# Performance work log

Measured on AMD Instinct MI355X. Metric: run time of the kernel, lower is better.

## Reference

```python
import jax, jax.numpy as jnp
import numpy as np

N_BASIS = 5  # identity, transpose, diag-embed(diag), row-sum broadcast, total-sum broadcast


def eq2to2_ops(x):
    """x: [B, d, n, n] -> [B, 5, d, n, n] equivariant basis ops (sums normalized by n, n^2)."""
    n = x.shape[-1]
    eye = jnp.eye(n, dtype=x.dtype)
    xt = jnp.swapaxes(x, -1, -2)
    diag = jnp.diagonal(x, axis1=-2, axis2=-1)            # [B, d, n]
    diag_emb = diag[..., :, None] * eye                   # [B, d, n, n]
    row = jnp.broadcast_to(x.sum(-1, keepdims=True) / n, x.shape)
    tot = jnp.broadcast_to(x.sum((-2, -1), keepdims=True) / (n * n), x.shape)
    return jnp.stack([x, xt, diag_emb, row, tot], axis=1)


def eq_layer(x, W, b):
    """x: [B, d_in, n, n]; W: [d_in, d_out, 5]; b: [d_out] -> [B, d_out, n, n]."""
    ops = eq2to2_ops(x)                                   # [B, 5, d_in, n, n]
    return jnp.einsum('bqdij,dsq->bsij', ops, W) + b[None, :, None, None]


def setup_inputs() -> dict:
    key = jax.random.key(0)
    ks = jax.random.split(key, 8)
    B, n, nin, nhid, ndechid, nout = 8, 256, 16, 32, 128, 1
    s = lambda fan: 1.0 / np.sqrt(fan)
    return {
        'x': jax.random.normal(ks[0], (B, n, nin), jnp.float32),
        'W1': jax.random.normal(ks[1], (2 * nin, nhid, N_BASIS), jnp.float32) * s(2 * nin * N_BASIS),
        'b1': jnp.zeros((nhid,), jnp.float32),
        'W2': jax.random.normal(ks[2], (nhid, nhid, N_BASIS), jnp.float32) * s(nhid * N_BASIS),
        'b2': jnp.zeros((nhid,), jnp.float32),
        'D1': jax.random.normal(ks[3], (nhid, ndechid), jnp.float32) * s(nhid),
        'db1': jnp.zeros((ndechid,), jnp.float32),
        'D2': jax.random.normal(ks[4], (ndechid, ndechid), jnp.float32) * s(ndechid),
        'db2': jnp.zeros((ndechid,), jnp.float32),
        'D3': jax.random.normal(ks[5], (ndechid, nout), jnp.float32) * s(ndechid),
        'db3': jnp.zeros((nout,), jnp.float32),
    }


def reference(x, W1, b1, W2, b2, D1, db1, D2, db2, D3, db3):
    B, n, d = x.shape
    eye = jnp.eye(n, dtype=x.dtype)
    # diag_embed(x.permute(0,2,1)) -> [B, d, n, n]
    x1 = jnp.swapaxes(x, 1, 2)[..., :, None] * eye
    # outer-product pairwise interactions -> [B, d, n, n]
    x2 = jnp.einsum('bid,bjd->bdij', x, x)
    h = jnp.concatenate([x1, x2], axis=1)                 # [B, 2d, n, n]
    h = jax.nn.relu(eq_layer(h, W1, b1))
    h = jax.nn.relu(eq_layer(h, W2, b2))
    h = jax.nn.relu(h.sum((-2, -1)))                      # [B, nhid]
    h = jax.nn.relu(h @ D1 + db1)
    h = jax.nn.relu(h @ D2 + db2)
    return h @ D3 + db3
```

## Files before the change

kernel.cpp:

```cpp
#include <hip/hip_runtime.h>
#include <hip/hip_bf16.h>


#define NB 8
#define NN 256
#define ND 16
#define NC 32
#define W1S (NC * 5)

using bf16x8 = __attribute__((ext_vector_type(8))) __bf16;
using f32x4  = __attribute__((ext_vector_type(4))) float;

#define MFMA(a, b, c) __builtin_amdgcn_mfma_f32_16x16x32_bf16((a), (b), (c), 0, 0, 0)

__global__ __launch_bounds__(256) void kB_pre(
    const float* __restrict__ x, const float* __restrict__ W1,
    const float* __restrict__ b1, const float* __restrict__ W2,
    float* __restrict__ S, float* __restrict__ T1,
    float* __restrict__ Tot1, float* __restrict__ G,
    float* __restrict__ W2dT, float* __restrict__ W2rT, float* __restrict__ W2tT,
    __bf16* __restrict__ A1wT, __bf16* __restrict__ WpT, __bf16* __restrict__ WmT)
{
    int b = blockIdx.x, t = threadIdx.x;
    __shared__ float part[16][ND + 1];
    __shared__ float sS[ND];
    const float* xb = x + b * NN * ND;

    { int i0 = t >> 4, d = t & 15; float p = 0.f;
      #pragma unroll
      for (int k = 0; k < 16; ++k) p += xb[(i0 + (k << 4)) * ND + d];
      part[i0][d] = p; }
    __syncthreads();
    if (t < ND) { float s = 0.f;
      #pragma unroll
      for (int k = 0; k < 16; ++k) s += part[k][t];
      sS[t] = s; S[b * ND + t] = s; }
    __syncthreads();
    if (t < NC) { int c = t; float tt = 0.f;
      #pragma unroll
      for (int d = 0; d < ND; ++d)
        tt += sS[d] * W1[d * W1S + c * 5 + 4]
            + sS[d] * sS[d] * W1[(ND + d) * W1S + c * 5 + 4];
      T1[b * NC + c] = tt * (1.f / 65536.f) + b1[c];
      Tot1[b * NC + c] = 0.f; G[b * NC + c] = 0.f; }
    if (b == 0) {
      for (int k = t; k < NC * ND; k += 256) {
        int c = k >> 4, d = k & 15;
        A1wT[k] = (__bf16)(W1[(ND + d) * W1S + c * 5 + 0]
                         + W1[(ND + d) * W1S + c * 5 + 1]);
      }
      for (int k = t; k < NC * NC; k += 256) {
        int s = k >> 5, c = k & 31;
        const float* w = W2 + c * W1S + s * 5;
        float w0 = w[0], w1 = w[1];
        WpT[k] = (__bf16)((w0 + w1) * 0.5f);
        WmT[k] = (__bf16)((w0 - w1) * 0.5f);
        W2dT[k] = w[2]; W2rT[k] = w[3]; W2tT[k] = w[4];
      }
    }
}

__global__ __launch_bounds__(256) void kC_rows(
    const float* __restrict__ x, const float* __restrict__ W1,
    const float* __restrict__ Sg, const float* __restrict__ T1g,
    const __bf16* __restrict__ A1wT,
    const float* __restrict__ W2dT, const float* __restrict__ W2rT,
    float* __restrict__ R1, float* __restrict__ Dg1, float* __restrict__ Tot1,
    float* __restrict__ CD2, float* __restrict__ CR2)
{
    const int i = blockIdx.x, b = blockIdx.y, t = threadIdx.x;
    __shared__ __align__(16) float  sX[NN][ND];
    __shared__ __align__(16) __bf16 sPA[NN][40];
    __shared__ __align__(16) __bf16 sBQ[NC][40];
    __shared__ float sS[ND], sDg[NC], sDiag[NC], sRow[NC];
    __shared__ float red[4][NC];

    { const float4* xb4 = (const float4*)(x + b * NN * ND);
      float4* sX4 = (float4*)&sX[0][0];
      #pragma unroll
      for (int kk = 0; kk < 4; ++kk) sX4[t + kk * 256] = xb4[t + kk * 256]; }
    if (t < ND) sS[t] = Sg[b * ND + t];
    for (int kk = 0; kk < 2; ++kk) {
      int idx = t + kk * 256; int c = idx >> 4, k = idx & 15;
      sBQ[c][k] = A1wT[idx];
    }
    __syncthreads();

    if (t < NC) {
      int c = t; float r = 0.f, dg = 0.f;
      #pragma unroll
      for (int d = 0; d < ND; ++d) {
        float xi = sX[i][d];
        r  += xi * W1[d * W1S + c * 5 + 3]
            + xi * sS[d] * W1[(ND + d) * W1S + c * 5 + 3];
        dg += xi * (W1[d * W1S + c * 5 + 0] + W1[d * W1S + c * 5 + 1]
                  + W1[d * W1S + c * 5 + 2])
            + xi * xi * W1[(ND + d) * W1S + c * 5 + 2];
      }
      r *= (1.f / 256.f);
      R1[(b * NN + i) * NC + c] = r;
      Dg1[(b * NN + i) * NC + c] = dg;
      sDg[c] = dg;
      sBQ[c][16] = (__bf16)(T1g[b * NC + c] + r);
      #pragma unroll
      for (int k = 17; k < 32; ++k) sBQ[c][k] = (__bf16)0.f;
    }
    {
      #pragma unroll
      for (int d = 0; d < ND; ++d) sPA[t][d] = (__bf16)(sX[i][d] * sX[t][d]);
      sPA[t][16] = (__bf16)1.f;
      #pragma unroll
      for (int k = 17; k < 32; ++k) sPA[t][k] = (__bf16)0.f;
    }
    __syncthreads();

    const int wv = t >> 6, ln = t & 63;
    const int m = ln & 15, quad = ln >> 4;
    const int c0 = m, c1 = m + 16;
    f32x4 zero = {0.f, 0.f, 0.f, 0.f};
    bf16x8 bq0 = *(const bf16x8*)&sBQ[c0][8 * quad];
    bf16x8 bq1 = *(const bf16x8*)&sBQ[c1][8 * quad];
    float rsum0 = 0.f, rsum1 = 0.f;
    #pragma unroll
    for (int gg = 0; gg < 4; ++gg) {
      int g = wv * 4 + gg;
      bf16x8 av = *(const bf16x8*)&sPA[g * 16 + m][8 * quad];
      f32x4 q0 = MFMA(av, bq0, zero);
      f32x4 q1 = MFMA(av, bq1, zero);
      #pragma unroll
      for (int r = 0; r < 4; ++r) {
        int pos = g * 16 + quad * 4 + r;
        float v0 = q0[r], v1 = q1[r];
        if (pos == i) { v0 += sDg[c0]; v1 += sDg[c1]; }
        float h0 = fmaxf(v0, 0.f), h1 = fmaxf(v1, 0.f);
        if (pos == i) { sDiag[c0] = h0; sDiag[c1] = h1; }
        rsum0 += h0; rsum1 += h1;
      }
    }
    rsum0 += __shfl_down(rsum0, 32, 64); rsum0 += __shfl_down(rsum0, 16, 64);
    rsum1 += __shfl_down(rsum1, 32, 64); rsum1 += __shfl_down(rsum1, 16, 64);
    if (ln < 16) { red[wv][ln] = rsum0; red[wv][ln + 16] = rsum1; }
    __syncthreads();
    if (t < NC) {
      float Row = red[0][t] + red[1][t] + red[2][t] + red[3][t];
      sRow[t] = Row;
      atomicAdd(&Tot1[b * NC + t], Row);
    }
    __syncthreads();
    if (t < NC) {
      int s = t; float cd = 0.f, cr = 0.f;
      #pragma unroll
      for (int c = 0; c < NC; ++c) {
        cd += sDiag[c] * W2dT[s * NC + c];
        cr += sRow[c]  * W2rT[s * NC + c];
      }
      CD2[(b * NN + i) * NC + s] = cd;
      CR2[(b * NN + i) * NC + s] = cr * (1.f / 256.f);
    }
}

__global__ __launch_bounds__(256) void kD_main(
    const float* __restrict__ x, const float* __restrict__ R1g,
    const float* __restrict__ Dg1g, const float* __restrict__ T1g,
    const float* __restrict__ CD2g, const float* __restrict__ CR2g,
    const float* __restrict__ Tot1g, const float* __restrict__ W2tT,
    const float* __restrict__ b2,
    const __bf16* __restrict__ A1wT, const __bf16* __restrict__ WpT,
    const __bf16* __restrict__ WmT,
    float* __restrict__ G)
{
    const int b = blockIdx.y, t = threadIdx.x;
    int TI = 0, rem = blockIdx.x;
    while (rem >= 16 - TI) { rem -= 16 - TI; ++TI; }
    const int TJ = TI + rem;
    const bool diagblk = (TI == TJ), mirror = (TI != TJ);

    __shared__ __align__(16) __bf16 sPA[NN][40];
    __shared__ __align__(16) __bf16 sV[NN][40];
    __shared__ __align__(16) __bf16 sBQ[NC][40];
    __shared__ __align__(16) __bf16 sWp[NC][40];
    __shared__ __align__(16) __bf16 sWm[NC][40];
    __shared__ float sXI[16][ND], sXJ[16][ND];
    __shared__ float sR1I[16][NC], sR1J[16][NC];
    __shared__ float sCR2I[16][NC], sCR2J[16][NC];
    __shared__ float sCD2I[16][NC], sDgI[16][NC];
    __shared__ float sCT2[NC];
    __shared__ float red[4][NC];

    { int r = t >> 4, d = t & 15;
      sXI[r][d] = x[(b * NN + TI * 16 + r) * ND + d];
      sXJ[r][d] = x[(b * NN + TJ * 16 + r) * ND + d]; }
    #pragma unroll
    for (int kk = 0; kk < 2; ++kk) {
      int idx = t + kk * 256; int r = idx >> 5, c = idx & 31;
      sR1I[r][c]  = R1g [(b * NN + TI * 16 + r) * NC + c];
      sR1J[r][c]  = R1g [(b * NN + TJ * 16 + r) * NC + c];
      sCR2I[r][c] = CR2g[(b * NN + TI * 16 + r) * NC + c];
      sCR2J[r][c] = CR2g[(b * NN + TJ * 16 + r) * NC + c];
      sCD2I[r][c] = CD2g[(b * NN + TI * 16 + r) * NC + c];
      sDgI[r][c]  = Dg1g[(b * NN + TI * 16 + r) * NC + c];
    }
    #pragma unroll
    for (int kk = 0; kk < 2; ++kk) {
      int idx = t + kk * 256; int c = idx >> 4, k = idx & 15;
      sBQ[c][k] = A1wT[idx];
    }
    if (t < NC) {
      sBQ[t][16] = (__bf16)T1g[b * NC + t];
      #pragma unroll
      for (int k = 17; k < 32; ++k) sBQ[t][k] = (__bf16)0.f;
    }
    #pragma unroll
    for (int kk = 0; kk < 4; ++kk) {
      int idx = t + kk * 256; int s = idx >> 5, c = idx & 31;
      sWp[s][c] = WpT[idx]; sWm[s][c] = WmT[idx];
    }
    if (t < NC) {
      float ct = 0.f;
      #pragma unroll
      for (int c = 0; c < NC; ++c) ct += Tot1g[b * NC + c] * W2tT[t * NC + c];
      sCT2[t] = ct * (1.f / 65536.f) + b2[t];
    }
    __syncthreads();

    {
      int ti = t >> 4, tj = t & 15;
      #pragma unroll
      for (int d = 0; d < ND; ++d) sPA[t][d] = (__bf16)(sXI[ti][d] * sXJ[tj][d]);
      sPA[t][16] = (__bf16)1.f;
      #pragma unroll
      for (int k = 17; k < 32; ++k) sPA[t][k] = (__bf16)0.f;
    }
    __syncthreads();

    const int wv = t >> 6, ln = t & 63;
    const int m = ln & 15, quad = ln >> 4;
    const int c0 = m, c1 = m + 16;
    f32x4 zero = {0.f, 0.f, 0.f, 0.f};

    {
      bf16x8 bq0 = *(const bf16x8*)&sBQ[c0][8 * quad];
      bf16x8 bq1 = *(const bf16x8*)&sBQ[c1][8 * quad];
      #pragma unroll
      for (int gg = 0; gg < 4; ++gg) {
        int g = wv * 4 + gg;
        bf16x8 av = *(const bf16x8*)&sPA[g * 16 + m][8 * quad];
        f32x4 q0 = MFMA(av, bq0, zero);
        f32x4 q1 = MFMA(av, bq1, zero);
        float r1i0 = sR1I[g][c0], r1i1 = sR1I[g][c1];
        #pragma unroll
        for (int r = 0; r < 4; ++r) {
          int tj = quad * 4 + r;
          float a0 = q0[r] + r1i0, b0 = q0[r] + sR1J[tj][c0];
          float a1v = q1[r] + r1i1, b1v = q1[r] + sR1J[tj][c1];
          if (diagblk && tj == g) {
            a0 += sDgI[g][c0]; b0 = a0;
            a1v += sDgI[g][c1]; b1v = a1v;
          }
          float hA0 = fmaxf(a0, 0.f), hB0 = fmaxf(b0, 0.f);
          float hA1 = fmaxf(a1v, 0.f), hB1 = fmaxf(b1v, 0.f);
          int pos = g * 16 + tj;
          sPA[pos][c0] = (__bf16)(hA0 + hB0);  sV[pos][c0] = (__bf16)(hA0 - hB0);
          sPA[pos][c1] = (__bf16)(hA1 + hB1);  sV[pos][c1] = (__bf16)(hA1 - hB1);
        }
      }
    }
    __syncthreads();

    const int s0 = m, s1 = m + 16;
    bf16x8 wp0 = *(const bf16x8*)&sWp[s0][8 * quad];
    bf16x8 wp1 = *(const bf16x8*)&sWp[s1][8 * quad];
    bf16x8 wm0 = *(const bf16x8*)&sWm[s0][8 * quad];
    bf16x8 wm1 = *(const bf16x8*)&sWm[s1][8 * quad];
    float ct0 = sCT2[s0], ct1 = sCT2[s1];
    float acc0 = 0.f, acc1 = 0.f;
    #pragma unroll
    for (int gg = 0; gg < 4; ++gg) {
      int g = wv * 4 + gg;
      bf16x8 ua = *(const bf16x8*)&sPA[g * 16 + m][8 * quad];
      bf16x8 va = *(const bf16x8*)&sV [g * 16 + m][8 * quad];
      f32x4 P0 = MFMA(ua, wp0, zero);
      f32x4 M0 = MFMA(va, wm0, zero);
      f32x4 P1 = MFMA(ua, wp1, zero);
      f32x4 M1 = MFMA(va, wm1, zero);
      float crI0 = sCR2I[g][s0], crI1 = sCR2I[g][s1];
      float cd0 = sCD2I[g][s0],  cd1 = sCD2I[g][s1];
      #pragma unroll
      for (int r = 0; r < 4; ++r) {
        int tj = quad * 4 + r;
        float a1 = P0[r] + M0[r] + crI0 + ct0;
        float a2 = P0[r] - M0[r] + sCR2J[tj][s0] + ct0;
        float b1v = P1[r] + M1[r] + crI1 + ct1;
        float b2v = P1[r] - M1[r] + sCR2J[tj][s1] + ct1;
        if (diagblk && tj == g) { a1 += cd0; b1v += cd1; }
        acc0 += fmaxf(a1, 0.f); acc1 += fmaxf(b1v, 0.f);
        if (mirror) { acc0 += fmaxf(a2, 0.f); acc1 += fmaxf(b2v, 0.f); }
      }
    }
    acc0 += __shfl_down(acc0, 32, 64); acc0 += __shfl_down(acc0, 16, 64);
    acc1 += __shfl_down(acc1, 32, 64); acc1 += __shfl_down(acc1, 16, 64);
    if (ln < 16) { red[wv][ln] = acc0; red[wv][ln + 16] = acc1; }
    __syncthreads();
    if (t < NC) {
      float v = red[0][t] + red[1][t] + red[2][t] + red[3][t];
      atomicAdd(&G[b * NC + t], v);
    }
}

__global__ __launch_bounds__(128) void k5_mlp(
    const float* __restrict__ G, const float* __restrict__ D1, const float* __restrict__ db1,
    const float* __restrict__ D2, const float* __restrict__ db2,
    const float* __restrict__ D3, const float* __restrict__ db3,
    float* __restrict__ out)
{
    int b = blockIdx.x, t = threadIdx.x;
    __shared__ float a[NC], h2s[128], r2[2];
    if (t < NC) a[t] = fmaxf(G[b * NC + t], 0.f);
    __syncthreads();
    float acc = db1[t];
    #pragma unroll
    for (int s = 0; s < NC; ++s) acc += a[s] * D1[s * 128 + t];
    float h2 = fmaxf(acc, 0.f);
    h2s[t] = h2;
    __syncthreads();
    float acc2 = db2[t];
    for (int u = 0; u < 128; ++u) acc2 += h2s[u] * D2[u * 128 + t];
    float h3 = fmaxf(acc2, 0.f);
    float v = h3 * D3[t];
    #pragma unroll
    for (int off = 32; off > 0; off >>= 1) v += __shfl_down(v, off, 64);
    if ((t & 63) == 0) r2[t >> 6] = v;
    __syncthreads();
    if (t == 0) out[b] = r2[0] + r2[1] + db3[0];
}

extern "C" void kernel_launch(void* const* d_in, const int* in_sizes, int n_in,
                              void* d_out, int out_size, void* d_ws, size_t ws_size,
                              hipStream_t stream)
{
    const float* x   = (const float*)d_in[0];
    const float* W1  = (const float*)d_in[1];
    const float* b1  = (const float*)d_in[2];
    const float* W2  = (const float*)d_in[3];
    const float* b2  = (const float*)d_in[4];
    const float* D1  = (const float*)d_in[5];
    const float* db1 = (const float*)d_in[6];
    const float* D2  = (const float*)d_in[7];
    const float* db2 = (const float*)d_in[8];
    const float* D3  = (const float*)d_in[9];
    const float* db3 = (const float*)d_in[10];
    float* out = (float*)d_out;

    float* w = (float*)d_ws;
    float* pS    = w; w += NB * ND;
    float* pT1   = w; w += NB * NC;
    float* pTot1 = w; w += NB * NC;
    float* pG    = w; w += NB * NC;
    float* pR1   = w; w += NB * NN * NC;
    float* pDg1  = w; w += NB * NN * NC;
    float* pCD2  = w; w += NB * NN * NC;
    float* pCR2  = w; w += NB * NN * NC;
    float* pW2d  = w; w += NC * NC;
    float* pW2r  = w; w += NC * NC;
    float* pW2t  = w; w += NC * NC;
    __bf16* bw = (__bf16*)w;
    __bf16* pA1wT = bw; bw += NC * ND;
    __bf16* pWpT  = bw; bw += NC * NC;
    __bf16* pWmT  = bw; bw += NC * NC;

    hipLaunchKernelGGL(kB_pre, dim3(NB), dim3(256), 0, stream,
                       x, W1, b1, W2, pS, pT1, pTot1, pG,
                       pW2d, pW2r, pW2t, pA1wT, pWpT, pWmT);
    hipLaunchKernelGGL(kC_rows, dim3(NN, NB), dim3(256), 0, stream,
                       x, W1, pS, pT1, pA1wT, pW2d, pW2r,
                       pR1, pDg1, pTot1, pCD2, pCR2);
    hipLaunchKernelGGL(kD_main, dim3(136, NB), dim3(256), 0, stream,
                       x, pR1, pDg1, pT1, pCD2, pCR2, pTot1, pW2t, b2,
                       pA1wT, pWpT, pWmT, pG);
    hipLaunchKernelGGL(k5_mlp, dim3(NB), dim3(128), 0, stream,
                       pG, D1, db1, D2, db2, D3, db3, out);
}
```

Before: 123.2 us.

## Fuse preprocessing into row kernel, batch 8 rows per block, replace atomics with partials

Removes the separate preprocessing kernel by recomputing column sums, T1 and the bf16 weight transforms inside the row and main kernels. The row kernel now handles 8 rows per block (32 blocks per batch instead of 256), looping over column chunks with MFMA. Global atomics are replaced by per-block partial buffers that later kernels reduce, which also drops the need to zero accumulators. This trades one kernel launch and the atomic traffic for redundant per-block weight and sum recomputation, plus fewer, longer-running row blocks.

```diff
diff --git a/kernel.cpp b/kernel.cpp
--- a/kernel.cpp
+++ b/kernel.cpp
@@ -6,185 +6,201 @@
 #define NN 256
 #define ND 16
 #define NC 32
-#define W1S (NC * 5)
+#define W1S 160
+#define W2S 160
 
 using bf16x8 = __attribute__((ext_vector_type(8))) __bf16;
 using f32x4  = __attribute__((ext_vector_type(4))) float;
 
 #define MFMA(a, b, c) __builtin_amdgcn_mfma_f32_16x16x32_bf16((a), (b), (c), 0, 0, 0)
 
-__global__ __launch_bounds__(256) void kB_pre(
+__global__ __launch_bounds__(256) void kC_rows(
     const float* __restrict__ x, const float* __restrict__ W1,
     const float* __restrict__ b1, const float* __restrict__ W2,
-    float* __restrict__ S, float* __restrict__ T1,
-    float* __restrict__ Tot1, float* __restrict__ G,
-    float* __restrict__ W2dT, float* __restrict__ W2rT, float* __restrict__ W2tT,
-    __bf16* __restrict__ A1wT, __bf16* __restrict__ WpT, __bf16* __restrict__ WmT)
+    float* __restrict__ T1g, float* __restrict__ R1, float* __restrict__ Dg1,
+    float* __restrict__ TotP, float* __restrict__ CD2, float* __restrict__ CR2)
 {
-    int b = blockIdx.x, t = threadIdx.x;
+    const int TI = blockIdx.x, b = blockIdx.y, t = threadIdx.x;
+    __shared__ __align__(16) float  sX[NN][ND + 1];
+    __shared__ __align__(16) __bf16 sP[NN][40];
+    __shared__ __align__(16) __bf16 sBQ[NC][48];
     __shared__ float part[16][ND + 1];
-    __shared__ float sS[ND];
-    const float* xb = x + b * NN * ND;
-
-    { int i0 = t >> 4, d = t & 15; float p = 0.f;
-      #pragma unroll
-      for (int k = 0; k < 16; ++k) p += xb[(i0 + (k << 4)) * ND + d];
-      part[i0][d] = p; }
-    __syncthreads();
-    if (t < ND) { float s = 0.f;
-      #pragma unroll
-      for (int k = 0; k < 16; ++k) s += part[k][t];
-      sS[t] = s; S[b * ND + t] = s; }
-    __syncthreads();
-    if (t < NC) { int c = t; float tt = 0.f;
-      #pragma unroll
-      for (int d = 0; d < ND; ++d)
-        tt += sS[d] * W1[d * W1S + c * 5 + 4]
-            + sS[d] * sS[d] * W1[(ND + d) * W1S + c * 5 + 4];
-      T1[b * NC + c] = tt * (1.f / 65536.f) + b1[c];
-      Tot1[b * NC + c] = 0.f; G[b * NC + c] = 0.f; }
-    if (b == 0) {
-      for (int k = t; k < NC * ND; k += 256) {
-        int c = k >> 4, d = k & 15;
-        A1wT[k] = (__bf16)(W1[(ND + d) * W1S + c * 5 + 0]
-                         + W1[(ND + d) * W1S + c * 5 + 1]);
-      }
-      for (int k = t; k < NC * NC; k += 256) {
-        int s = k >> 5, c = k & 31;
-        const float* w = W2 + c * W1S + s * 5;
-        float w0 = w[0], w1 = w[1];
-        WpT[k] = (__bf16)((w0 + w1) * 0.5f);
-        WmT[k] = (__bf16)((w0 - w1) * 0.5f);
-        W2dT[k] = w[2]; W2rT[k] = w[3]; W2tT[k] = w[4];
-      }
+    __shared__ float sS[ND], sT1[NC];
+    __shared__ float sRT[8][NC], sDgL[8][NC], sRow[8][NC], sDiag[8][NC];
+
+    const float* xg = x + b * NN * ND;
+    #pragma unroll
+    for (int kk = 0; kk < 16; ++kk) {
+        int idx = t + kk * 256;
+        sX[idx >> 4][idx & 15] = xg[idx];
+    }
+    #pragma unroll
+    for (int kk = 0; kk < 2; ++kk) {
+        int idx = t + kk * 256;
+        int c = idx >> 4, k = idx & 15;
+        sBQ[c][k] = (__bf16)(W1[(ND + k) * W1S + c * 5 + 0]
+                           + W1[(ND + k) * W1S + c * 5 + 1]);
+    }
+    #pragma unroll
+    for (int kk = 0; kk < 4; ++kk) {
+        int idx = t + kk * 256;
+        sBQ[idx >> 5][16 + (idx & 31)] = (__bf16)0.f;
+    }
+    {
+        uint32_t* z = (uint32_t*)&sP[0][0];
+        #pragma unroll
+        for (int kk = 0; kk < 8; ++kk) {
+            int idx = t + kk * 256;
+            z[(idx >> 3) * 20 + 8 + (idx & 7)] = 0u;
+        }
+    }
+    __syncthreads();
+
+    {
+        int rr = t >> 4, d = t & 15;
+        float p = 0.f;
+        #pragma unroll
+        for (int k = 0; k < 16; ++k) p += sX[rr + (k << 4)][d];
+        part[rr][d] = p;
+    }
+    __syncthreads();
+    if (t < ND) {
+        float s = 0.f;
+        #pragma unroll
+        for (int k = 0; k < 16; ++k) s += part[k][t];
+        sS[t] = s;
+    }
+    __syncthreads();
+    if (t < NC) {
+        int c = t; float tt = 0.f;
+        #pragma unroll
+        for (int d = 0; d < ND; ++d)
+            tt += sS[d] * W1[d * W1S + c * 5 + 4]
+                + sS[d] * sS[d] * W1[(ND + d) * W1S + c * 5 + 4];
+        float v = tt * (1.f / 65536.f) + b1[c];
+        sT1[c] = v;
+        if (TI == 0) T1g[b * NC + c] = v;
+    }
+    __syncthreads();
+    {
+        int i_l = t >> 5, c = t & 31;
+        int gi = TI * 8 + i_l;
+        float r = 0.f, dg = 0.f;
+        #pragma unroll
+        for (int d = 0; d < ND; ++d) {
+            float xi = sX[gi][d];
+            const float* wa = W1 + d * W1S + c * 5;
+            const float* wb = W1 + (ND + d) * W1S + c * 5;
+            r  += xi * wa[3] + xi * sS[d] * wb[3];
+            dg += xi * (wa[0] + wa[1] + wa[2]) + xi * xi * wb[2];
+        }
+        r *= (1.f / 256.f);
+        R1[(b * NN + gi) * NC + c] = r;
+        Dg1[(b * NN + gi) * NC + c] = dg;
+        sRT[i_l][c] = sT1[c] + r;
+        sDgL[i_l][c] = dg;
+    }
+
+    const int ln = t & 63, wv = t >> 6;
+    const int m = ln & 15, quad = ln >> 4;
+    bf16x8 bq0 = *(const bf16x8*)&sBQ[m][8 * quad];
+    bf16x8 bq1 = *(const bf16x8*)&sBQ[m + 16][8 * quad];
+    f32x4 zero = {0.f, 0.f, 0.f, 0.f};
+    float rs0[4] = {0.f, 0.f, 0.f, 0.f}, rs1[4] = {0.f, 0.f, 0.f, 0.f};
+    const int i_base = TI * 8;
+
+    for (int jg = 0; jg < 8; ++jg) {
+        __syncthreads();
+        {
+            int i_l = t >> 5, j_l = t & 31;
+            const float* xi = &sX[i_base + i_l][0];
+            const float* xj = &sX[jg * 32 + j_l][0];
+            bf16x8 v0, v1;
+            #pragma unroll
+            for (int d = 0; d < 8; ++d) v0[d] = (__bf16)(xi[d] * xj[d]);
+            #pragma unroll
+            for (int d = 0; d < 8; ++d) v1[d] = (__bf16)(xi[8 + d] * xj[8 + d]);
+            *(bf16x8*)&sP[t][0] = v0;
+            *(bf16x8*)&sP[t][8] = v1;
+        }
+        __syncthreads();
+        #pragma unroll
+        for (int gg = 0; gg < 4; ++gg) {
+            int g = wv * 4 + gg;
+            bf16x8 av = *(const bf16x8*)&sP[g * 16 + m][8 * quad];
+            f32x4 q0 = MFMA(av, bq0, zero);
+            f32x4 q1 = MFMA(av, bq1, zero);
+            int i_l = g >> 1;
+            int gi = i_base + i_l;
+            float rt0 = sRT[i_l][m], rt1 = sRT[i_l][m + 16];
+            int jb = jg * 32 + (g & 1) * 16 + quad * 4;
+            #pragma unroll
+            for (int r = 0; r < 4; ++r) {
+                float v0 = q0[r] + rt0, v1 = q1[r] + rt1;
+                bool dgf = (jb + r == gi);
+                if (dgf) { v0 += sDgL[i_l][m]; v1 += sDgL[i_l][m + 16]; }
+                float h0 = fmaxf(v0, 0.f), h1 = fmaxf(v1, 0.f);
+                if (dgf) { sDiag[i_l][m] = h0; sDiag[i_l][m + 16] = h1; }
+                rs0[gg] += h0; rs1[gg] += h1;
+            }
+        }
+    }
+    float a0 = rs0[0] + rs0[1], a1 = rs0[2] + rs0[3];
+    float b0 = rs1[0] + rs1[1], b1v = rs1[2] + rs1[3];
+    a0 += __shfl_down(a0, 32, 64);  a0 += __shfl_down(a0, 16, 64);
+    a1 += __shfl_down(a1, 32, 64);  a1 += __shfl_down(a1, 16, 64);
+    b0 += __shfl_down(b0, 32, 64);  b0 += __shfl_down(b0, 16, 64);
+    b1v += __shfl_down(b1v, 32, 64); b1v += __shfl_down(b1v, 16, 64);
+    __syncthreads();
+    if (ln < 16) {
+        sRow[wv * 2][ln] = a0;       sRow[wv * 2 + 1][ln] = a1;
+        sRow[wv * 2][ln + 16] = b0;  sRow[wv * 2 + 1][ln + 16] = b1v;
+    }
+    __syncthreads();
+    if (t < NC) {
+        float s = 0.f;
+        #pragma unroll
+        for (int i = 0; i < 8; ++i) s += sRow[i][t];
+        TotP[TI * (NB * NC) + b * NC + t] = s;
+    }
+    {
+        int i_l = t >> 5, s = t & 31;
+        int gi = i_base + i_l;
+        float cd = 0.f, cr = 0.f;
+        #pragma unroll
+        for (int c = 0; c < NC; ++c) {
+            cd += sDiag[i_l][c] * W2[c * W2S + s * 5 + 2];
+            cr += sRow[i_l][c]  * W2[c * W2S + s * 5 + 3];
+        }
+        CD2[(b * NN + gi) * NC + s] = cd;
+        CR2[(b * NN + gi) * NC + s] = cr * (1.f / 256.f);
     }
 }
 
-__global__ __launch_bounds__(256) void kC_rows(
+__global__ __launch_bounds__(256) void kD_main(
     const float* __restrict__ x, const float* __restrict__ W1,
-    const float* __restrict__ Sg, const float* __restrict__ T1g,
-    const __bf16* __restrict__ A1wT,
-    const float* __restrict__ W2dT, const float* __restrict__ W2rT,
-    float* __restrict__ R1, float* __restrict__ Dg1, float* __restrict__ Tot1,
-    float* __restrict__ CD2, float* __restrict__ CR2)
-{
-    const int i = blockIdx.x, b = blockIdx.y, t = threadIdx.x;
-    __shared__ __align__(16) float  sX[NN][ND];
-    __shared__ __align__(16) __bf16 sPA[NN][40];
-    __shared__ __align__(16) __bf16 sBQ[NC][40];
-    __shared__ float sS[ND], sDg[NC], sDiag[NC], sRow[NC];
-    __shared__ float red[4][NC];
-
-    { const float4* xb4 = (const float4*)(x + b * NN * ND);
-      float4* sX4 = (float4*)&sX[0][0];
-      #pragma unroll
-      for (int kk = 0; kk < 4; ++kk) sX4[t + kk * 256] = xb4[t + kk * 256]; }
-    if (t < ND) sS[t] = Sg[b * ND + t];
-    for (int kk = 0; kk < 2; ++kk) {
-      int idx = t + kk * 256; int c = idx >> 4, k = idx & 15;
-      sBQ[c][k] = A1wT[idx];
-    }
-    __syncthreads();
-
-    if (t < NC) {
-      int c = t; float r = 0.f, dg = 0.f;
-      #pragma unroll
-      for (int d = 0; d < ND; ++d) {
-        float xi = sX[i][d];
-        r  += xi * W1[d * W1S + c * 5 + 3]
-            + xi * sS[d] * W1[(ND + d) * W1S + c * 5 + 3];
-        dg += xi * (W1[d * W1S + c * 5 + 0] + W1[d * W1S + c * 5 + 1]
-                  + W1[d * W1S + c * 5 + 2])
-            + xi * xi * W1[(ND + d) * W1S + c * 5 + 2];
-      }
-      r *= (1.f / 256.f);
-      R1[(b * NN + i) * NC + c] = r;
-      Dg1[(b * NN + i) * NC + c] = dg;
-      sDg[c] = dg;
-      sBQ[c][16] = (__bf16)(T1g[b * NC + c] + r);
-      #pragma unroll
-      for (int k = 17; k < 32; ++k) sBQ[c][k] = (__bf16)0.f;
-    }
-    {
-      #pragma unroll
-      for (int d = 0; d < ND; ++d) sPA[t][d] = (__bf16)(sX[i][d] * sX[t][d]);
-      sPA[t][16] = (__bf16)1.f;
-      #pragma unroll
-      for (int k = 17; k < 32; ++k) sPA[t][k] = (__bf16)0.f;
-    }
-    __syncthreads();
-
-    const int wv = t >> 6, ln = t & 63;
-    const int m = ln & 15, quad = ln >> 4;
-    const int c0 = m, c1 = m + 16;
-    f32x4 zero = {0.f, 0.f, 0.f, 0.f};
-    bf16x8 bq0 = *(const bf16x8*)&sBQ[c0][8 * quad];
-    bf16x8 bq1 = *(const bf16x8*)&sBQ[c1][8 * quad];
-    float rsum0 = 0.f, rsum1 = 0.f;
-    #pragma unroll
-    for (int gg = 0; gg < 4; ++gg) {
-      int g = wv * 4 + gg;
-      bf16x8 av = *(const bf16x8*)&sPA[g * 16 + m][8 * quad];
-      f32x4 q0 = MFMA(av, bq0, zero);
-      f32x4 q1 = MFMA(av, bq1, zero);
-      #pragma unroll
-      for (int r = 0; r < 4; ++r) {
-        int pos = g * 16 + quad * 4 + r;
-        float v0 = q0[r], v1 = q1[r];
-        if (pos == i) { v0 += sDg[c0]; v1 += sDg[c1]; }
-        float h0 = fmaxf(v0, 0.f), h1 = fmaxf(v1, 0.f);
-        if (pos == i) { sDiag[c0] = h0; sDiag[c1] = h1; }
-        rsum0 += h0; rsum1 += h1;
-      }
-    }
-    rsum0 += __shfl_down(rsum0, 32, 64); rsum0 += __shfl_down(rsum0, 16, 64);
-    rsum1 += __shfl_down(rsum1, 32, 64); rsum1 += __shfl_down(rsum1, 16, 64);
-    if (ln < 16) { red[wv][ln] = rsum0; red[wv][ln + 16] = rsum1; }
-    __syncthreads();
-    if (t < NC) {
-      float Row = red[0][t] + red[1][t] + red[2][t] + red[3][t];
-      sRow[t] = Row;
-      atomicAdd(&Tot1[b * NC + t], Row);
-    }
-    __syncthreads();
-    if (t < NC) {
-      int s = t; float cd = 0.f, cr = 0.f;
-      #pragma unroll
-      for (int c = 0; c < NC; ++c) {
-        cd += sDiag[c] * W2dT[s * NC + c];
-        cr += sRow[c]  * W2rT[s * NC + c];
-      }
-      CD2[(b * NN + i) * NC + s] = cd;
-      CR2[(b * NN + i) * NC + s] = cr * (1.f / 256.f);
-    }
-}
-
-__global__ __launch_bounds__(256) void kD_main(
-    const float* __restrict__ x, const float* __restrict__ R1g,
-    const float* __restrict__ Dg1g, const float* __restrict__ T1g,
-    const float* __restrict__ CD2g, const float* __restrict__ CR2g,
-    const float* __restrict__ Tot1g, const float* __restrict__ W2tT,
-    const float* __restrict__ b2,
-    const __bf16* __restrict__ A1wT, const __bf16* __restrict__ WpT,
-    const __bf16* __restrict__ WmT,
-    float* __restrict__ G)
+    const float* __restrict__ W2, const float* __restrict__ b2,
+    const float* __restrict__ T1g, const float* __restrict__ R1g,
+    const float* __restrict__ Dg1g, const float* __restrict__ CD2g,
+    const float* __restrict__ CR2g, const float* __restrict__ TotP,
+    float* __restrict__ GP)
 {
     const int b = blockIdx.y, t = threadIdx.x;
     int TI = 0, rem = blockIdx.x;
     while (rem >= 16 - TI) { rem -= 16 - TI; ++TI; }
     const int TJ = TI + rem;
-    const bool diagblk = (TI == TJ), mirror = (TI != TJ);
+    const bool diagblk = (TI == TJ), mirror = !diagblk;
 
     __shared__ __align__(16) __bf16 sPA[NN][40];
     __shared__ __align__(16) __bf16 sV[NN][40];
-    __shared__ __align__(16) __bf16 sBQ[NC][40];
+    __shared__ __align__(16) __bf16 sBQ[NC][48];
     __shared__ __align__(16) __bf16 sWp[NC][40];
     __shared__ __align__(16) __bf16 sWm[NC][40];
-    __shared__ float sXI[16][ND], sXJ[16][ND];
+    __shared__ float sXI[16][ND + 1], sXJ[16][ND + 1];
     __shared__ float sR1I[16][NC], sR1J[16][NC];
     __shared__ float sCR2I[16][NC], sCR2J[16][NC];
     __shared__ float sCD2I[16][NC], sDgI[16][NC];
-    __shared__ float sCT2[NC];
+    __shared__ float sT1[NC], sTot[NC], sCT2[NC];
     __shared__ float red[4][NC];
 
     { int r = t >> 4, d = t & 15;
@@ -203,33 +219,49 @@
     #pragma unroll
     for (int kk = 0; kk < 2; ++kk) {
       int idx = t + kk * 256; int c = idx >> 4, k = idx & 15;
-      sBQ[c][k] = A1wT[idx];
-    }
-    if (t < NC) {
-      sBQ[t][16] = (__bf16)T1g[b * NC + t];
-      #pragma unroll
-      for (int k = 17; k < 32; ++k) sBQ[t][k] = (__bf16)0.f;
+      sBQ[c][k] = (__bf16)(W1[(ND + k) * W1S + c * 5 + 0]
+                         + W1[(ND + k) * W1S + c * 5 + 1]);
+    }
+    #pragma unroll
+    for (int kk = 0; kk < 4; ++kk) {
+      int idx = t + kk * 256;
+      sBQ[idx >> 5][16 + (idx & 31)] = (__bf16)0.f;
     }
     #pragma unroll
     for (int kk = 0; kk < 4; ++kk) {
       int idx = t + kk * 256; int s = idx >> 5, c = idx & 31;
-      sWp[s][c] = WpT[idx]; sWm[s][c] = WmT[idx];
+      float w0 = W2[c * W2S + s * 5 + 0], w1 = W2[c * W2S + s * 5 + 1];
+      sWp[s][c] = (__bf16)((w0 + w1) * 0.5f);
+      sWm[s][c] = (__bf16)((w0 - w1) * 0.5f);
+    }
+    if (t < NC) {
+      sT1[t] = T1g[b * NC + t];
+      float tot = 0.f;
+      #pragma unroll
+      for (int k = 0; k < 32; ++k) tot += TotP[k * (NB * NC) + b * NC + t];
+      sTot[t] = tot;
+    }
+    __syncthreads();
+
+    {
+      int ti = t >> 4, tj = t & 15;
+      bf16x8 v0, v1, zv;
+      #pragma unroll
+      for (int d = 0; d < 8; ++d) {
+        v0[d] = (__bf16)(sXI[ti][d] * sXJ[tj][d]);
+        v1[d] = (__bf16)(sXI[ti][8 + d] * sXJ[tj][8 + d]);
+        zv[d] = (__bf16)0.f;
+      }
+      *(bf16x8*)&sPA[t][0]  = v0;
+      *(bf16x8*)&sPA[t][8]  = v1;
+      *(bf16x8*)&sPA[t][16] = zv;
+      *(bf16x8*)&sPA[t][24] = zv;
     }
     if (t < NC) {
       float ct = 0.f;
       #pragma unroll
-      for (int c = 0; c < NC; ++c) ct += Tot1g[b * NC + c] * W2tT[t * NC + c];
+      for (int c = 0; c < NC; ++c) ct += sTot[c] * W2[c * W2S + t * 5 + 4];
       sCT2[t] = ct * (1.f / 65536.f) + b2[t];
-    }
-    __syncthreads();
-
-    {
-      int ti = t >> 4, tj = t & 15;
-      #pragma unroll
-      for (int d = 0; d < ND; ++d) sPA[t][d] = (__bf16)(sXI[ti][d] * sXJ[tj][d]);
-      sPA[t][16] = (__bf16)1.f;
-      #pragma unroll
-      for (int k = 17; k < 32; ++k) sPA[t][k] = (__bf16)0.f;
     }
     __syncthreads();
 
@@ -241,18 +273,19 @@
     {
       bf16x8 bq0 = *(const bf16x8*)&sBQ[c0][8 * quad];
       bf16x8 bq1 = *(const bf16x8*)&sBQ[c1][8 * quad];
+      float t10 = sT1[c0], t11 = sT1[c1];
       #pragma unroll
       for (int gg = 0; gg < 4; ++gg) {
         int g = wv * 4 + gg;
         bf16x8 av = *(const bf16x8*)&sPA[g * 16 + m][8 * quad];
         f32x4 q0 = MFMA(av, bq0, zero);
         f32x4 q1 = MFMA(av, bq1, zero);
-        float r1i0 = sR1I[g][c0], r1i1 = sR1I[g][c1];
+        float r1i0 = sR1I[g][c0] + t10, r1i1 = sR1I[g][c1] + t11;
         #pragma unroll
         for (int r = 0; r < 4; ++r) {
           int tj = quad * 4 + r;
-          float a0 = q0[r] + r1i0, b0 = q0[r] + sR1J[tj][c0];
-          float a1v = q1[r] + r1i1, b1v = q1[r] + sR1J[tj][c1];
+          float a0 = q0[r] + r1i0, b0 = q0[r] + sR1J[tj][c0] + t10;
+          float a1v = q1[r] + r1i1, b1v = q1[r] + sR1J[tj][c1] + t11;
           if (diagblk && tj == g) {
             a0 += sDgI[g][c0]; b0 = a0;
             a1v += sDgI[g][c1]; b1v = a1v;
@@ -283,18 +316,18 @@
       f32x4 M0 = MFMA(va, wm0, zero);
       f32x4 P1 = MFMA(ua, wp1, zero);
       f32x4 M1 = MFMA(va, wm1, zero);
-      float crI0 = sCR2I[g][s0], crI1 = sCR2I[g][s1];
-      float cd0 = sCD2I[g][s0],  cd1 = sCD2I[g][s1];
+      float crI0 = sCR2I[g][s0] + ct0, crI1 = sCR2I[g][s1] + ct1;
+      float cd0 = sCD2I[g][s0], cd1 = sCD2I[g][s1];
       #pragma unroll
       for (int r = 0; r < 4; ++r) {
         int tj = quad * 4 + r;
-        float a1 = P0[r] + M0[r] + crI0 + ct0;
+        float a1 = P0[r] + M0[r] + crI0;
         float a2 = P0[r] - M0[r] + sCR2J[tj][s0] + ct0;
-        float b1v = P1[r] + M1[r] + crI1 + ct1;
-        float b2v = P1[r] - M1[r] + sCR2J[tj][s1] + ct1;
-        if (diagblk && tj == g) { a1 += cd0; b1v += cd1; }
-        acc0 += fmaxf(a1, 0.f); acc1 += fmaxf(b1v, 0.f);
-        if (mirror) { acc0 += fmaxf(a2, 0.f); acc1 += fmaxf(b2v, 0.f); }
+        float e1 = P1[r] + M1[r] + crI1;
+        float e2 = P1[r] - M1[r] + sCR2J[tj][s1] + ct1;
+        if (diagblk && tj == g) { a1 += cd0; e1 += cd1; }
+        acc0 += fmaxf(a1, 0.f); acc1 += fmaxf(e1, 0.f);
+        if (mirror) { acc0 += fmaxf(a2, 0.f); acc1 += fmaxf(e2, 0.f); }
       }
     }
     acc0 += __shfl_down(acc0, 32, 64); acc0 += __shfl_down(acc0, 16, 64);
@@ -302,20 +335,27 @@
     if (ln < 16) { red[wv][ln] = acc0; red[wv][ln + 16] = acc1; }
     __syncthreads();
     if (t < NC) {
-      float v = red[0][t] + red[1][t] + red[2][t] + red[3][t];
-      atomicAdd(&G[b * NC + t], v);
+      GP[blockIdx.x * (NB * NC) + b * NC + t]
+          = red[0][t] + red[1][t] + red[2][t] + red[3][t];
     }
 }
 
 __global__ __launch_bounds__(128) void k5_mlp(
-    const float* __restrict__ G, const float* __restrict__ D1, const float* __restrict__ db1,
-    const float* __restrict__ D2, const float* __restrict__ db2,
-    const float* __restrict__ D3, const float* __restrict__ db3,
-    float* __restrict__ out)
+    const float* __restrict__ GP, const float* __restrict__ D1,
+    const float* __restrict__ db1, const float* __restrict__ D2,
+    const float* __restrict__ db2, const float* __restrict__ D3,
+    const float* __restrict__ db3, float* __restrict__ out)
 {
     int b = blockIdx.x, t = threadIdx.x;
-    __shared__ float a[NC], h2s[128], r2[2];
-    if (t < NC) a[t] = fmaxf(G[b * NC + t], 0.f);
+    __shared__ float sGp[4][NC], a[NC], h2s[128], r2[2];
+    {
+        int q = t >> 5, s = t & 31;
+        float p = 0.f;
+        for (int k = q; k < 136; k += 4) p += GP[k * (NB * NC) + b * NC + s];
+        sGp[q][s] = p;
+    }
+    __syncthreads();
+    if (t < NC) a[t] = fmaxf(sGp[0][t] + sGp[1][t] + sGp[2][t] + sGp[3][t], 0.f);
     __syncthreads();
     float acc = db1[t];
     #pragma unroll
@@ -352,31 +392,18 @@
     float* out = (float*)d_out;
 
     float* w = (float*)d_ws;
-    float* pS    = w; w += NB * ND;
     float* pT1   = w; w += NB * NC;
-    float* pTot1 = w; w += NB * NC;
-    float* pG    = w; w += NB * NC;
+    float* pTotP = w; w += 32 * NB * NC;
+    float* pGP   = w; w += 136 * NB * NC;
     float* pR1   = w; w += NB * NN * NC;
     float* pDg1  = w; w += NB * NN * NC;
     float* pCD2  = w; w += NB * NN * NC;
     float* pCR2  = w; w += NB * NN * NC;
-    float* pW2d  = w; w += NC * NC;
-    float* pW2r  = w; w += NC * NC;
-    float* pW2t  = w; w += NC * NC;
-    __bf16* bw = (__bf16*)w;
-    __bf16* pA1wT = bw; bw += NC * ND;
-    __bf16* pWpT  = bw; bw += NC * NC;
-    __bf16* pWmT  = bw; bw += NC * NC;
-
-    hipLaunchKernelGGL(kB_pre, dim3(NB), dim3(256), 0, stream,
-                       x, W1, b1, W2, pS, pT1, pTot1, pG,
-                       pW2d, pW2r, pW2t, pA1wT, pWpT, pWmT);
-    hipLaunchKernelGGL(kC_rows, dim3(NN, NB), dim3(256), 0, stream,
-                       x, W1, pS, pT1, pA1wT, pW2d, pW2r,
-                       pR1, pDg1, pTot1, pCD2, pCR2);
+
+    hipLaunchKernelGGL(kC_rows, dim3(32, NB), dim3(256), 0, stream,
+                       x, W1, b1, W2, pT1, pR1, pDg1, pTotP, pCD2, pCR2);
     hipLaunchKernelGGL(kD_main, dim3(136, NB), dim3(256), 0, stream,
-                       x, pR1, pDg1, pT1, pCD2, pCR2, pTot1, pW2t, b2,
-                       pA1wT, pWpT, pWmT, pG);
+                       x, W1, W2, b2, pT1, pR1, pDg1, pCD2, pCR2, pTotP, pGP);
     hipLaunchKernelGGL(k5_mlp, dim3(NB), dim3(128), 0, stream,
-                       pG, D1, db1, D2, db2, D3, db3, out);
+                       pGP, D1, db1, D2, db2, D3, db3, out);
 }
```

Result: faster. 119.2 us (-3.2%).
